# Optimization experiments

Hardware: AMD Instinct MI355X
Metric: run time of the kernel (lower is better)

## Reference

```python
import jax, jax.numpy as jnp
import numpy as np

N_NODES = 50000
N_EDGES = 800000
N_GRAPHS = 1000
IN_F = 11
H = 128
BN_EPS = 1e-5


def _bn(h, g, b):
    # BatchNorm1d training-mode math (biased variance), no running stats
    m = h.mean(axis=0)
    v = h.var(axis=0)
    return (h - m) * jax.lax.rsqrt(v + BN_EPS) * g + b


def _mlp(h, w1, b1, g1, be1, w2, b2, g2, be2):
    h = jax.nn.relu(_bn(h @ w1 + b1, g1, be1))
    h = jax.nn.relu(_bn(h @ w2 + b2, g2, be2))
    return h


def _gin_agg(h, edge_index):
    # GINConv with eps=0: (1+eps)*x + sum_{j->i} x_j
    msgs = h[edge_index[0]]  # [E, F] gather
    agg = jax.ops.segment_sum(msgs, edge_index[1], num_segments=N_NODES)
    return h + agg


def setup_inputs() -> dict:
    key = jax.random.key(0)
    ks = jax.random.split(key, 24)
    d = {}
    d["x"] = jax.random.normal(ks[0], (N_NODES, IN_F), dtype=jnp.float32)
    d["edge_index"] = jax.random.randint(ks[1], (2, N_EDGES), 0, N_NODES, dtype=jnp.int64)
    d["batch"] = jnp.sort(jax.random.randint(ks[2], (N_NODES,), 0, N_GRAPHS, dtype=jnp.int64))

    dims = [
        ("l1", IN_F, H), ("l2", H, H),            # conv1 MLP
        ("l3", H, 2 * H), ("l4", 2 * H, 2 * H),    # conv2 MLP
        ("l5", 2 * H, 2 * H), ("l6", 2 * H, 2 * H),# conv3 MLP
    ]
    ki = 3
    for name, fi, fo in dims:
        d[name + "w"] = jax.random.normal(ks[ki], (fi, fo), dtype=jnp.float32) * (1.0 / np.sqrt(fi)); ki += 1
        d[name + "b"] = jax.random.normal(ks[ki], (fo,), dtype=jnp.float32) * 0.02; ki += 1
        d[name + "g"] = 1.0 + jax.random.normal(ks[ki], (fo,), dtype=jnp.float32) * 0.02; ki += 1
        d[name + "be"] = jax.random.normal(ks[ki], (fo,), dtype=jnp.float32) * 0.02; ki += 1
        ks = jax.random.split(ks[-1], 24); ki = 0
    d["fw1"] = jax.random.normal(ks[0], (2 * H, H), dtype=jnp.float32) * (1.0 / np.sqrt(2 * H))
    d["fb1"] = jax.random.normal(ks[1], (H,), dtype=jnp.float32) * 0.02
    d["fg"] = 1.0 + jax.random.normal(ks[2], (H,), dtype=jnp.float32) * 0.02
    d["fbe"] = jax.random.normal(ks[3], (H,), dtype=jnp.float32) * 0.02
    d["fw2"] = jax.random.normal(ks[4], (H, 1), dtype=jnp.float32) * (1.0 / np.sqrt(H))
    d["fb2"] = jax.random.normal(ks[5], (1,), dtype=jnp.float32) * 0.02
    return d


def reference(x, edge_index, batch,
              l1w, l1b, l1g, l1be, l2w, l2b, l2g, l2be,
              l3w, l3b, l3g, l3be, l4w, l4b, l4g, l4be,
              l5w, l5b, l5g, l5be, l6w, l6b, l6g, l6be,
              fw1, fb1, fg, fbe, fw2, fb2):
    # conv1 + relu (dropout = identity in eval)
    h = _mlp(_gin_agg(x, edge_index), l1w, l1b, l1g, l1be, l2w, l2b, l2g, l2be)
    h = jax.nn.relu(h)
    # conv2 + relu
    h = _mlp(_gin_agg(h, edge_index), l3w, l3b, l3g, l3be, l4w, l4b, l4g, l4be)
    h = jax.nn.relu(h)
    # conv3 + relu
    h = _mlp(_gin_agg(h, edge_index), l5w, l5b, l5g, l5be, l6w, l6b, l6g, l6be)
    h = jax.nn.relu(h)
    # global_add_pool over graphs
    hg = jax.ops.segment_sum(h, batch, num_segments=N_GRAPHS)  # [G, 256]
    hg = jax.nn.relu(_bn(hg @ fw1 + fb1, fg, fbe))
    out = hg @ fw2 + fb2  # [G, 1]
    return out.reshape(-1)
```

## Files before the change

kernel.cpp:

```cpp
#include <hip/hip_runtime.h>

#define NNODES 50000
#define NEDGES 800000
#define NGRAPHS 1000
#define BN_EPS 1e-5f
#define MPAD 50048

typedef unsigned short us_t;
typedef us_t us8 __attribute__((ext_vector_type(8)));
typedef us_t us4 __attribute__((ext_vector_type(4)));
typedef __bf16 bf16x8 __attribute__((ext_vector_type(8)));
typedef float f32x4 __attribute__((ext_vector_type(4)));

__device__ __forceinline__ float b2f(us_t u) {
    union { unsigned int i; float f; } v;
    v.i = ((unsigned int)u) << 16;
    return v.f;
}
__device__ __forceinline__ us_t f2b(float x) {
    unsigned int u = __float_as_uint(x);
    unsigned int r = u + 0x7FFFu + ((u >> 16) & 1u);
    return (us_t)(r >> 16);
}
__device__ __forceinline__ float h2f(us_t u) {
    _Float16 h;
    __builtin_memcpy(&h, &u, 2);
    return (float)h;
}
__device__ __forceinline__ us_t f2h(float x) {
    _Float16 h = (_Float16)x;
    us_t u;
    __builtin_memcpy(&u, &h, 2);
    return u;
}
__device__ __forceinline__ bf16x8 as_bf(us8 v) {
    union { us8 u; bf16x8 b; } c;
    c.u = v;
    return c.b;
}

__device__ __forceinline__ void glds16(const us_t* g, us_t* l) {
    __builtin_amdgcn_global_load_lds(
        (const __attribute__((address_space(1))) void*)g,
        (__attribute__((address_space(3))) void*)l, 16, 0, 0);
}


__global__ void zero_f32(float* __restrict__ p, int n) {
    int i = blockIdx.x * blockDim.x + threadIdx.x;
    if (i < n) p[i] = 0.f;
}


__global__ void csr_hist(const int* __restrict__ dst, int* __restrict__ deg, int E) {
    int e = blockIdx.x * blockDim.x + threadIdx.x;
    if (e < E) atomicAdd(&deg[dst[e]], 1);
}

__global__ void csr_scan1(const int* __restrict__ deg, int* __restrict__ tmpscan,
                          int* __restrict__ chunkTot, int n) {
    __shared__ int sm[1024];
    int i = blockIdx.x * 1024 + threadIdx.x;
    int v = (i < n) ? deg[i] : 0;
    sm[threadIdx.x] = v;
    __syncthreads();
    for (int off = 1; off < 1024; off <<= 1) {
        int add = (threadIdx.x >= off) ? sm[threadIdx.x - off] : 0;
        __syncthreads();
        sm[threadIdx.x] += add;
        __syncthreads();
    }
    if (i < n) tmpscan[i] = sm[threadIdx.x];
    if (threadIdx.x == 1023) chunkTot[blockIdx.x] = sm[1023];
}

__global__ void csr_scan2(int* __restrict__ chunkTot, int nchunks) {
    if (threadIdx.x == 0 && blockIdx.x == 0) {
        int run = 0;
        for (int c = 0; c < nchunks; c++) {
            int t = chunkTot[c];
            chunkTot[c] = run;
            run += t;
        }
    }
}

__global__ void csr_scan3(const int* __restrict__ deg, const int* __restrict__ tmpscan,
                          const int* __restrict__ chunkTot, int* __restrict__ rowptr,
                          int* __restrict__ cursor, int n) {
    int i = blockIdx.x * blockDim.x + threadIdx.x;
    if (i < n) {
        int inc = tmpscan[i] + chunkTot[i >> 10];
        rowptr[i + 1] = inc;
        cursor[i] = inc - deg[i];
        if (i == 0) rowptr[0] = 0;
    }
}

__global__ void csr_fill(const int* __restrict__ src, const int* __restrict__ dst,
                         int* __restrict__ cursor, int* __restrict__ eidx, int E) {
    int e = blockIdx.x * blockDim.x + threadIdx.x;
    if (e < E) {
        int pos = atomicAdd(&cursor[dst[e]], 1);
        eidx[pos] = src[e];
    }
}


__global__ void wt_convert_all(const float* __restrict__ w2, const float* __restrict__ w3,
                               const float* __restrict__ w4, const float* __restrict__ w5,
                               const float* __restrict__ w6,
                               us_t* __restrict__ o2, us_t* __restrict__ o3,
                               us_t* __restrict__ o4, us_t* __restrict__ o5,
                               us_t* __restrict__ o6) {
    int i = blockIdx.x * blockDim.x + threadIdx.x;
    if (i < 16384) {
        int k = i >> 7, n = i & 127;
        o2[n * 128 + k] = f2b(w2[i]);
    } else if (i < 49152) {
        int j = i - 16384; int k = j >> 8, n = j & 255;
        o3[n * 128 + k] = f2b(w3[j]);
    } else if (i < 114688) {
        int j = i - 49152; int k = j >> 8, n = j & 255;
        o4[n * 256 + k] = f2b(w4[j]);
    } else if (i < 180224) {
        int j = i - 114688; int k = j >> 8, n = j & 255;
        o5[n * 256 + k] = f2b(w5[j]);
    } else if (i < 245760) {
        int j = i - 180224; int k = j >> 8, n = j & 255;
        o6[n * 256 + k] = f2b(w6[j]);
    }
}


__global__ void gin_gather_bn128(const us_t* __restrict__ z, const float* __restrict__ sums,
                                 const float* __restrict__ sumsq, const float* __restrict__ gw,
                                 const float* __restrict__ bw, float invM,
                                 const int* __restrict__ rowptr, const int* __restrict__ eidx,
                                 us_t* __restrict__ out) {
    int ln = threadIdx.x >> 4;
    int fp = threadIdx.x & 15;
    int n = blockIdx.x * 16 + ln;
    if (n >= NNODES) return;
    int f0 = fp * 8;
    float s[8], t[8];
    #pragma unroll
    for (int q = 0; q < 8; q++) {
        float m = sums[f0 + q] * invM;
        float va = sumsq[f0 + q] * invM - m * m;
        s[q] = gw[f0 + q] * rsqrtf(va + BN_EPS);
        t[q] = bw[f0 + q] - m * s[q];
    }
    const us_t* zf = z + f0;
    float a[8];
    us8 v = *(const us8*)&zf[(size_t)n * 128];
    #pragma unroll
    for (int q = 0; q < 8; q++) a[q] = fmaxf(0.f, b2f(v[q]) * s[q] + t[q]);
    int p0 = rowptr[n], p1 = rowptr[n + 1];
    int p = p0;
    for (; p + 4 <= p1; p += 4) {
        int e0 = eidx[p], e1 = eidx[p + 1], e2 = eidx[p + 2], e3 = eidx[p + 3];
        us8 u0 = *(const us8*)&zf[(size_t)e0 * 128];
        us8 u1 = *(const us8*)&zf[(size_t)e1 * 128];
        us8 u2 = *(const us8*)&zf[(size_t)e2 * 128];
        us8 u3 = *(const us8*)&zf[(size_t)e3 * 128];
        #pragma unroll
        for (int q = 0; q < 8; q++)
            a[q] += fmaxf(0.f, b2f(u0[q]) * s[q] + t[q]) +
                    fmaxf(0.f, b2f(u1[q]) * s[q] + t[q]) +
                    fmaxf(0.f, b2f(u2[q]) * s[q] + t[q]) +
                    fmaxf(0.f, b2f(u3[q]) * s[q] + t[q]);
    }
    for (; p < p1; p++) {
        us8 u = *(const us8*)&zf[(size_t)eidx[p] * 128];
        #pragma unroll
        for (int q = 0; q < 8; q++) a[q] += fmaxf(0.f, b2f(u[q]) * s[q] + t[q]);
    }
    us8 o;
    #pragma unroll
    for (int q = 0; q < 8; q++) o[q] = f2b(a[q]);
    *(us8*)&out[(size_t)n * 128 + f0] = o;
}


__global__ void gin_gather_bn256(const us_t* __restrict__ z, const float* __restrict__ sums,
                                 const float* __restrict__ sumsq, const float* __restrict__ gw,
                                 const float* __restrict__ bw, float invM,
                                 const int* __restrict__ rowptr, const int* __restrict__ eidx,
                                 us_t* __restrict__ out) {
    int ln = threadIdx.x >> 5;
    int fp = threadIdx.x & 31;
    int n = blockIdx.x * 8 + ln;
    if (n >= NNODES) return;
    int f0 = fp * 8;
    float s[8], t[8];
    #pragma unroll
    for (int q = 0; q < 8; q++) {
        float m = sums[f0 + q] * invM;
        float va = sumsq[f0 + q] * invM - m * m;
        s[q] = gw[f0 + q] * rsqrtf(va + BN_EPS);
        t[q] = bw[f0 + q] - m * s[q];
    }
    const us_t* zf = z + f0;
    float a[8];
    us8 v = *(const us8*)&zf[(size_t)n * 256];
    #pragma unroll
    for (int q = 0; q < 8; q++) a[q] = fmaxf(0.f, b2f(v[q]) * s[q] + t[q]);
    int p0 = rowptr[n], p1 = rowptr[n + 1];
    int p = p0;
    for (; p + 4 <= p1; p += 4) {
        int e0 = eidx[p], e1 = eidx[p + 1], e2 = eidx[p + 2], e3 = eidx[p + 3];
        us8 u0 = *(const us8*)&zf[(size_t)e0 * 256];
        us8 u1 = *(const us8*)&zf[(size_t)e1 * 256];
        us8 u2 = *(const us8*)&zf[(size_t)e2 * 256];
        us8 u3 = *(const us8*)&zf[(size_t)e3 * 256];
        #pragma unroll
        for (int q = 0; q < 8; q++)
            a[q] += fmaxf(0.f, b2f(u0[q]) * s[q] + t[q]) +
                    fmaxf(0.f, b2f(u1[q]) * s[q] + t[q]) +
                    fmaxf(0.f, b2f(u2[q]) * s[q] + t[q]) +
                    fmaxf(0.f, b2f(u3[q]) * s[q] + t[q]);
    }
    for (; p < p1; p++) {
        us8 u = *(const us8*)&zf[(size_t)eidx[p] * 256];
        #pragma unroll
        for (int q = 0; q < 8; q++) a[q] += fmaxf(0.f, b2f(u[q]) * s[q] + t[q]);
    }
    us8 o;
    #pragma unroll
    for (int q = 0; q < 8; q++) o[q] = f2b(a[q]);
    *(us8*)&out[(size_t)n * 256 + f0] = o;
}

__global__ void gin_gather11(const float* __restrict__ x, const int* __restrict__ rowptr,
                             const int* __restrict__ eidx, float* __restrict__ out) {
    int local = threadIdx.x >> 4;
    int lane = threadIdx.x & 15;
    int n = blockIdx.x * 16 + local;
    if (n >= NNODES) return;
    int p0 = rowptr[n], p1 = rowptr[n + 1];
    float acc = (lane < 11) ? x[n * 11 + lane] : 0.f;
    for (int p = p0; p < p1; p++) {
        int src = eidx[p];
        if (lane < 11) acc += x[src * 11 + lane];
    }
    if (lane < 11) out[n * 11 + lane] = acc;
}


__global__ __launch_bounds__(256) void gemm11(const float* __restrict__ A,
                                              const float* __restrict__ W,
                                              const float* __restrict__ b,
                                              us_t* __restrict__ C,
                                              float* __restrict__ sums,
                                              float* __restrict__ sumsq) {
    __shared__ float sW[11 * 128];
    __shared__ float sArows[64 * 11];
    int tid = threadIdx.x;
    for (int i = tid; i < 11 * 128; i += 256) sW[i] = W[i];
    int r0 = blockIdx.x * 64;
    for (int i = tid; i < 64 * 11; i += 256) {
        int r = i / 11, c = i - r * 11;
        sArows[i] = (r0 + r < NNODES) ? A[(r0 + r) * 11 + c] : 0.f;
    }
    __syncthreads();
    int col = tid & 127;
    int half = tid >> 7;
    float bias = b[col];
    float cs = 0.f, cq = 0.f;
    for (int rr = half * 32; rr < half * 32 + 32; rr++) {
        int row = r0 + rr;
        if (row < NNODES) {
            float acc = bias;
            #pragma unroll
            for (int k = 0; k < 11; k++) acc += sArows[rr * 11 + k] * sW[k * 128 + col];
            C[(size_t)row * 128 + col] = f2h(acc);
            cs += acc;
            cq += acc * acc;
        }
    }
    __syncthreads();
    sArows[tid] = cs;
    sArows[256 + tid] = cq;
    __syncthreads();
    if (tid < 128) {
        atomicAdd(&sums[tid], sArows[tid] + sArows[tid + 128]);
        atomicAdd(&sumsq[tid], sArows[256 + tid] + sArows[256 + tid + 128]);
    }
}


template <int K_, int AMODE, int OMODE, int COLS>
__global__ __launch_bounds__(256, 4) void gemm_v7(
    const void* __restrict__ Ap, const us_t* __restrict__ Wt,
    const float* __restrict__ bias,
    const float* __restrict__ sums_in, const float* __restrict__ sumsq_in,
    const float* __restrict__ gma, const float* __restrict__ bet, float invM,
    void* __restrict__ Cp, float* __restrict__ sums, float* __restrict__ sumsq,
    int M, int N, int nrows) {
    __shared__ us_t sA[128 * 32];
    __shared__ us_t sB[128 * 32];
    __shared__ float sST[(AMODE >= 1) ? 2 * K_ : 2];

    int rowblk, colblk;
    if (COLS == 1) {
        rowblk = blockIdx.x;
        colblk = 0;
    } else {
        int g = blockIdx.x;
        rowblk = (g >> 4) * 8 + (g & 7);
        colblk = (g >> 3) & 1;
        if (rowblk >= nrows) return;
    }
    const int bm = rowblk * 128;
    const int bn = colblk * 128;

    const int tid = threadIdx.x;
    const int lane = tid & 63;
    const int wave = tid >> 6;
    const int wm = wave >> 1, wn = wave & 1;
    const int lrow = lane & 15, lquad = lane >> 4;

    if (AMODE >= 1) {
        if (tid < K_) {
            float m = sums_in[tid] * invM;
            float va = sumsq_in[tid] * invM - m * m;
            float sc = gma[tid] * rsqrtf(va + BN_EPS);
            sST[tid] = sc;
            sST[K_ + tid] = bet[tid] - m * sc;
        }
        __syncthreads();
    }

    f32x4 acc[4][4] = {};

    const int r0c = tid >> 2, q0c = tid & 3;
    const int r1c = (tid + 256) >> 2, q1c = tid & 3;

    #pragma unroll
    for (int kt = 0; kt < K_ / 32; kt++) {
        const int k0 = kt * 32;

        us8 pk[2];
        if (AMODE >= 1) {
            #pragma unroll
            for (int i = 0; i < 2; i++) {
                int row = (i == 0) ? r0c : r1c;
                int kq = (i == 0) ? q0c : q1c;
                int kk = k0 + kq * 8;
                float v[8];
                if (AMODE == 1) {
                    const float* ar = &((const float*)Ap)[(size_t)(bm + row) * K_ + kk];
                    float4 v0 = *(const float4*)ar;
                    float4 v1 = *(const float4*)(ar + 4);
                    v[0] = v0.x; v[1] = v0.y; v[2] = v0.z; v[3] = v0.w;
                    v[4] = v1.x; v[5] = v1.y; v[6] = v1.z; v[7] = v1.w;
                } else {
                    us8 u = *(const us8*)&((const us_t*)Ap)[(size_t)(bm + row) * K_ + kk];
                    #pragma unroll
                    for (int q = 0; q < 8; q++) v[q] = h2f(u[q]);
                }
                float4 s0 = *(const float4*)&sST[kk];
                float4 s1 = *(const float4*)&sST[kk + 4];
                float4 t0 = *(const float4*)&sST[K_ + kk];
                float4 t1 = *(const float4*)&sST[K_ + kk + 4];
                us8 o;
                o[0] = f2b(fmaxf(0.f, v[0] * s0.x + t0.x));
                o[1] = f2b(fmaxf(0.f, v[1] * s0.y + t0.y));
                o[2] = f2b(fmaxf(0.f, v[2] * s0.z + t0.z));
                o[3] = f2b(fmaxf(0.f, v[3] * s0.w + t0.w));
                o[4] = f2b(fmaxf(0.f, v[4] * s1.x + t1.x));
                o[5] = f2b(fmaxf(0.f, v[5] * s1.y + t1.y));
                o[6] = f2b(fmaxf(0.f, v[6] * s1.z + t1.z));
                o[7] = f2b(fmaxf(0.f, v[7] * s1.w + t1.w));
                pk[i] = o;
            }
        }

        __syncthreads();

        {
            glds16(&Wt[(size_t)(bn + r0c) * K_ + k0 + q0c * 8], &sB[(wave * 64) * 8]);
            glds16(&Wt[(size_t)(bn + r1c) * K_ + k0 + q1c * 8], &sB[(256 + wave * 64) * 8]);
        }
        if (AMODE == 0) {
            const us_t* A = (const us_t*)Ap;
            glds16(&A[(size_t)(bm + r0c) * K_ + k0 + q0c * 8], &sA[(wave * 64) * 8]);
            glds16(&A[(size_t)(bm + r1c) * K_ + k0 + q1c * 8], &sA[(256 + wave * 64) * 8]);
        } else {
            *(us8*)&sA[(size_t)tid * 8] = pk[0];
            *(us8*)&sA[(size_t)(tid + 256) * 8] = pk[1];
        }

        __syncthreads();

        bf16x8 af[4], bfr[4];
        #pragma unroll
        for (int i = 0; i < 4; i++)
            af[i] = as_bf(*(const us8*)&sA[(wm * 64 + i * 16 + lrow) * 32 + lquad * 8]);
        #pragma unroll
        for (int j = 0; j < 4; j++)
            bfr[j] = as_bf(*(const us8*)&sB[(wn * 64 + j * 16 + lrow) * 32 + lquad * 8]);
        #pragma unroll
        for (int i = 0; i < 4; i++)
            #pragma unroll
            for (int j = 0; j < 4; j++)
                acc[i][j] = __builtin_amdgcn_mfma_f32_16x16x32_bf16(af[i], bfr[j],
                                                                    acc[i][j], 0, 0, 0);
    }

    #pragma unroll
    for (int j = 0; j < 4; j++) {
        int col = bn + wn * 64 + j * 16 + lrow;
        float bcol = bias[col];
        float cs = 0.f, cq = 0.f;
        #pragma unroll
        for (int i = 0; i < 4; i++) {
            int rb = bm + wm * 64 + i * 16 + lquad * 4;
            #pragma unroll
            for (int r = 0; r < 4; r++) {
                int row = rb + r;
                float zv = acc[i][j][r] + bcol;
                if (row < M) {
                    if (OMODE == 0)
                        ((us_t*)Cp)[(size_t)row * N + col] = f2b(zv);
                    else if (OMODE == 1)
                        ((float*)Cp)[(size_t)row * N + col] = zv;
                    else
                        ((us_t*)Cp)[(size_t)row * N + col] = f2h(zv);
                    cs += zv;
                    cq += zv * zv;
                }
            }
        }
        cs += __shfl_xor(cs, 16); cs += __shfl_xor(cs, 32);
        cq += __shfl_xor(cq, 16); cq += __shfl_xor(cq, 32);
        if (lquad == 0) {
            atomicAdd(&sums[col], cs);
            atomicAdd(&sumsq[col], cq);
        }
    }
}


__global__ void pool_bn_raw(const float* __restrict__ z, const float* __restrict__ sums,
                            const float* __restrict__ sumsq, const float* __restrict__ gw,
                            const float* __restrict__ bw, float invM,
                            const int* __restrict__ batch, float* __restrict__ hg) {
    int f = threadIdx.x;
    float m = sums[f] * invM;
    float va = sumsq[f] * invM - m * m;
    float sv = gw[f] * rsqrtf(va + BN_EPS);
    float tv = bw[f] - m * sv;
    int n0 = blockIdx.x * 32;
    int n1 = min(n0 + 32, NNODES);
    float acc = 0.f;
    int gc = batch[n0];
    for (int n = n0; n < n1; n++) {
        int g = batch[n];
        if (g != gc) {
            atomicAdd(&hg[gc * 256 + f], acc);
            acc = 0.f;
            gc = g;
        }
        acc += fmaxf(0.f, z[(size_t)n * 256 + f] * sv + tv);
    }
    atomicAdd(&hg[gc * 256 + f], acc);
}


#define GBM 128
#define GBN 128
#define GBK 16
#define LDA 132

__global__ __launch_bounds__(256) void gemm_f32_head(
    const float* __restrict__ A, const float* __restrict__ W, const float* __restrict__ bias,
    float* __restrict__ C, float* __restrict__ sums, float* __restrict__ sumsq,
    int M, int K, int N) {
    __shared__ float smem[2 * GBK * LDA];
    float* As = smem;
    float* Ws = smem + GBK * LDA;

    const int bm = blockIdx.y * GBM;
    const int bn = blockIdx.x * GBN;
    const int tid = threadIdx.x;
    const int tm = tid >> 4;
    const int tn = tid & 15;

    float acc[2][2][4][4] = {};

    for (int k0 = 0; k0 < K; k0 += GBK) {
        #pragma unroll
        for (int i = 0; i < 2; i++) {
            int id = tid + 256 * i;
            int row = id >> 2;
            int kq = id & 3;
            int gr = bm + row;
            int kk = k0 + kq * 4;
            float4 a4 = make_float4(0.f, 0.f, 0.f, 0.f);
            if (gr < M && kk < K) a4 = *(const float4*)&A[(size_t)gr * K + kk];
            As[(kq * 4 + 0) * LDA + row] = a4.x;
            As[(kq * 4 + 1) * LDA + row] = a4.y;
            As[(kq * 4 + 2) * LDA + row] = a4.z;
            As[(kq * 4 + 3) * LDA + row] = a4.w;
        }
        #pragma unroll
        for (int i = 0; i < 2; i++) {
            int id = tid + 256 * i;
            int kl = id >> 5;
            int c = id & 31;
            int kk = k0 + kl;
            float4 w4 = make_float4(0.f, 0.f, 0.f, 0.f);
            if (kk < K && bn + c * 4 < N) w4 = *(const float4*)&W[(size_t)kk * N + bn + c * 4];
            *(float4*)&Ws[kl * LDA + c * 4] = w4;
        }
        __syncthreads();
        #pragma unroll
        for (int k = 0; k < GBK; k++) {
            float4 a0 = *(float4*)&As[k * LDA + tm * 4];
            float4 a1 = *(float4*)&As[k * LDA + 64 + tm * 4];
            float4 w0 = *(float4*)&Ws[k * LDA + tn * 4];
            float4 w1 = *(float4*)&Ws[k * LDA + 64 + tn * 4];
            float ar[2][4] = {{a0.x, a0.y, a0.z, a0.w}, {a1.x, a1.y, a1.z, a1.w}};
            float wr[2][4] = {{w0.x, w0.y, w0.z, w0.w}, {w1.x, w1.y, w1.z, w1.w}};
            #pragma unroll
            for (int ri = 0; ri < 2; ri++)
                #pragma unroll
                for (int ci = 0; ci < 2; ci++)
                    #pragma unroll
                    for (int ii = 0; ii < 4; ii++)
                        #pragma unroll
                        for (int jj = 0; jj < 4; jj++)
                            acc[ri][ci][ii][jj] += ar[ri][ii] * wr[ci][jj];
        }
        __syncthreads();
    }

    float colsum[2][4] = {};
    float colsq[2][4] = {};
    #pragma unroll
    for (int ci = 0; ci < 2; ci++) {
        int colbase = bn + ci * 64 + tn * 4;
        if (colbase >= N) continue;
        float4 b4 = *(const float4*)&bias[colbase];
        float br[4] = {b4.x, b4.y, b4.z, b4.w};
        #pragma unroll
        for (int ri = 0; ri < 2; ri++) {
            #pragma unroll
            for (int ii = 0; ii < 4; ii++) {
                int row = bm + ri * 64 + tm * 4 + ii;
                if (row < M) {
                    float z0 = acc[ri][ci][ii][0] + br[0];
                    float z1 = acc[ri][ci][ii][1] + br[1];
                    float z2 = acc[ri][ci][ii][2] + br[2];
                    float z3 = acc[ri][ci][ii][3] + br[3];
                    *(float4*)&C[(size_t)row * N + colbase] = make_float4(z0, z1, z2, z3);
                    colsum[ci][0] += z0; colsq[ci][0] += z0 * z0;
                    colsum[ci][1] += z1; colsq[ci][1] += z1 * z1;
                    colsum[ci][2] += z2; colsq[ci][2] += z2 * z2;
                    colsum[ci][3] += z3; colsq[ci][3] += z3 * z3;
                }
            }
        }
    }
    __syncthreads();
    float* ps = smem;
    float* pq = smem + 2048;
    #pragma unroll
    for (int ci = 0; ci < 2; ci++)
        #pragma unroll
        for (int jj = 0; jj < 4; jj++) {
            int cl = ci * 64 + tn * 4 + jj;
            ps[tm * 128 + cl] = colsum[ci][jj];
            pq[tm * 128 + cl] = colsq[ci][jj];
        }
    __syncthreads();
    if (tid < 128 && bn + tid < N) {
        float s = 0.f, q = 0.f;
        #pragma unroll
        for (int i = 0; i < 16; i++) {
            s += ps[i * 128 + tid];
            q += pq[i * 128 + tid];
        }
        atomicAdd(&sums[bn + tid], s);
        atomicAdd(&sumsq[bn + tid], q);
    }
}


__global__ void final_gemv_raw(const float* __restrict__ hg2, const float* __restrict__ sums,
                               const float* __restrict__ sumsq, const float* __restrict__ gw,
                               const float* __restrict__ bw, float invM,
                               const float* __restrict__ fw2, const float* __restrict__ fb2,
                               float* __restrict__ out) {
    int g = blockIdx.x;
    int l = threadIdx.x;
    float m0 = sums[l] * invM, va0 = sumsq[l] * invM - m0 * m0;
    float s0 = gw[l] * rsqrtf(va0 + BN_EPS), t0 = bw[l] - m0 * s0;
    float m1 = sums[64 + l] * invM, va1 = sumsq[64 + l] * invM - m1 * m1;
    float s1 = gw[64 + l] * rsqrtf(va1 + BN_EPS), t1 = bw[64 + l] - m1 * s1;
    float a0 = fmaxf(0.f, hg2[g * 128 + l] * s0 + t0) * fw2[l];
    float a1 = fmaxf(0.f, hg2[g * 128 + 64 + l] * s1 + t1) * fw2[64 + l];
    float v = a0 + a1;
    #pragma unroll
    for (int o = 32; o > 0; o >>= 1) v += __shfl_down(v, o);
    if (l == 0) out[g] = v + fb2[0];
}


extern "C" void kernel_launch(void* const* d_in, const int* in_sizes, int n_in,
                              void* d_out, int out_size, void* d_ws, size_t ws_size,
                              hipStream_t stream) {
    const float* x = (const float*)d_in[0];
    const int* ei = (const int*)d_in[1];
    const int* batch = (const int*)d_in[2];
    const int* esrc = ei;
    const int* edst = ei + NEDGES;

    const float* l1w = (const float*)d_in[3],  *l1b = (const float*)d_in[4],
               * l1g = (const float*)d_in[5],  *l1be = (const float*)d_in[6];
    const float* l2w = (const float*)d_in[7],  *l2b = (const float*)d_in[8],
               * l2g = (const float*)d_in[9],  *l2be = (const float*)d_in[10];
    const float* l3w = (const float*)d_in[11], *l3b = (const float*)d_in[12],
               * l3g = (const float*)d_in[13], *l3be = (const float*)d_in[14];
    const float* l4w = (const float*)d_in[15], *l4b = (const float*)d_in[16],
               * l4g = (const float*)d_in[17], *l4be = (const float*)d_in[18];
    const float* l5w = (const float*)d_in[19], *l5b = (const float*)d_in[20],
               * l5g = (const float*)d_in[21], *l5be = (const float*)d_in[22];
    const float* l6w = (const float*)d_in[23], *l6b = (const float*)d_in[24],
               * l6g = (const float*)d_in[25], *l6be = (const float*)d_in[26];
    const float* fw1 = (const float*)d_in[27], *fb1 = (const float*)d_in[28],
               * fg  = (const float*)d_in[29], *fbe = (const float*)d_in[30];
    const float* fw2 = (const float*)d_in[31], *fb2 = (const float*)d_in[32];

    us_t* F0h = (us_t*)d_ws;
    float* F1 = (float*)(F0h + (size_t)MPAD * 256);
    us_t* Ba = (us_t*)F1;
    us_t* Bz = Ba + (size_t)MPAD * 256;
    us_t* wt2 = (us_t*)(F1 + (size_t)MPAD * 256);
    us_t* wt3 = wt2 + 128 * 128;
    us_t* wt4 = wt3 + 256 * 128;
    us_t* wt5 = wt4 + 256 * 256;
    us_t* wt6 = wt5 + 256 * 256;
    float* agg11 = (float*)(wt6 + 256 * 256);
    float* hg = agg11 + (size_t)NNODES * 11;
    float* hg2 = hg + NGRAPHS * 256;
    float* stats = hg2 + NGRAPHS * 128;
    int* deg = (int*)(stats + 7 * 512);
    int* rowptr = deg + (NNODES + 1);
    int* cursor = rowptr + (NNODES + 1);
    int* chunkTot = cursor + (NNODES + 1);
    int* tmpscan = chunkTot + 64;
    int* eidx = tmpscan + (NNODES + 1);

    {
        int zn = NGRAPHS * 256 + NGRAPHS * 128 + 7 * 512 + (NNODES + 1);
        zero_f32<<<(zn + 255) / 256, 256, 0, stream>>>(hg, zn);
    }

    csr_hist<<<(NEDGES + 255) / 256, 256, 0, stream>>>(edst, deg, NEDGES);
    int nchunks = (NNODES + 1023) / 1024;
    csr_scan1<<<nchunks, 1024, 0, stream>>>(deg, tmpscan, chunkTot, NNODES);
    csr_scan2<<<1, 64, 0, stream>>>(chunkTot, nchunks);
    csr_scan3<<<(NNODES + 255) / 256, 256, 0, stream>>>(deg, tmpscan, chunkTot, rowptr,
                                                        cursor, NNODES);
    csr_fill<<<(NEDGES + 255) / 256, 256, 0, stream>>>(esrc, edst, cursor, eidx, NEDGES);

    wt_convert_all<<<(245760 + 255) / 256, 256, 0, stream>>>(l2w, l3w, l4w, l5w, l6w,
                                                             wt2, wt3, wt4, wt5, wt6);

    auto st = [&](int i) { return stats + i * 512; };
    const float invN = 1.0f / (float)NNODES;
    const float invG = 1.0f / (float)NGRAPHS;
    const int NRB = MPAD / 128;
    const int NSWZ = ((NRB + 7) / 8) * 16;

    gin_gather11<<<(NNODES + 15) / 16, 256, 0, stream>>>(x, rowptr, eidx, agg11);
    gemm11<<<(NNODES + 63) / 64, 256, 0, stream>>>(agg11, l1w, l1b, F0h, st(0), st(0) + 256);
    gemm_v7<128, 2, 0, 1><<<NRB, 256, 0, stream>>>(
        F0h, wt2, l2b, st(0), st(0) + 256, l1g, l1be, invN,
        Bz, st(1), st(1) + 256, NNODES, 128, NRB);

    gin_gather_bn128<<<(NNODES + 15) / 16, 256, 0, stream>>>(
        Bz, st(1), st(1) + 256, l2g, l2be, invN, rowptr, eidx, Ba);
    gemm_v7<128, 0, 2, 2><<<NSWZ, 256, 0, stream>>>(
        Ba, wt3, l3b, nullptr, nullptr, nullptr, nullptr, 0.f,
        F0h, st(2), st(2) + 256, NNODES, 256, NRB);
    gemm_v7<256, 2, 0, 2><<<NSWZ, 256, 0, stream>>>(
        F0h, wt4, l4b, st(2), st(2) + 256, l3g, l3be, invN,
        Bz, st(3), st(3) + 256, NNODES, 256, NRB);

    gin_gather_bn256<<<(NNODES + 7) / 8, 256, 0, stream>>>(
        Bz, st(3), st(3) + 256, l4g, l4be, invN, rowptr, eidx, Ba);
    gemm_v7<256, 0, 2, 2><<<NSWZ, 256, 0, stream>>>(
        Ba, wt5, l5b, nullptr, nullptr, nullptr, nullptr, 0.f,
        F0h, st(4), st(4) + 256, NNODES, 256, NRB);
    gemm_v7<256, 2, 1, 2><<<NSWZ, 256, 0, stream>>>(
        F0h, wt6, l6b, st(4), st(4) + 256, l5g, l5be, invN,
        F1, st(5), st(5) + 256, NNODES, 256, NRB);

    pool_bn_raw<<<(NNODES + 31) / 32, 256, 0, stream>>>(
        F1, st(5), st(5) + 256, l6g, l6be, invN, batch, hg);
    gemm_f32_head<<<dim3(1, 8), 256, 0, stream>>>(hg, fw1, fb1, hg2, st(6), st(6) + 256,
                                                  NGRAPHS, 256, 128);
    final_gemv_raw<<<NGRAPHS, 64, 0, stream>>>(hg2, st(6), st(6) + 256, fg, fbe, invG,
                                               fw2, fb2, (float*)d_out);
}
```

Before: 626.9 us.

## Stage GEMM epilogue through LDS for vectorized stores; store last layer in fp16

The GEMM epilogue now writes the biased outputs into shared memory, one half-tile of 64 rows at a time, and then copies them out with 16-byte coalesced row stores. Before, each thread wrote scattered 2-byte elements straight to global memory. The last MLP layer now writes fp16 instead of fp32, so the pooling kernel reads half the bytes. The cost is two extra barriers per half-tile, LDS reuse, and lower precision on the final activations before BN and pooling.

```diff
diff --git a/kernel.cpp b/kernel.cpp
--- a/kernel.cpp
+++ b/kernel.cpp
@@ -291,16 +291,17 @@
 
 
 template <int K_, int AMODE, int OMODE, int COLS>
-__global__ __launch_bounds__(256, 4) void gemm_v7(
+__global__ __launch_bounds__(256, 4) void gemm_v8(
     const void* __restrict__ Ap, const us_t* __restrict__ Wt,
     const float* __restrict__ bias,
     const float* __restrict__ sums_in, const float* __restrict__ sumsq_in,
     const float* __restrict__ gma, const float* __restrict__ bet, float invM,
-    void* __restrict__ Cp, float* __restrict__ sums, float* __restrict__ sumsq,
+    us_t* __restrict__ Cp, float* __restrict__ sums, float* __restrict__ sumsq,
     int M, int N, int nrows) {
-    __shared__ us_t sA[128 * 32];
-    __shared__ us_t sB[128 * 32];
+    __shared__ us_t sAB[2 * 128 * 32];
     __shared__ float sST[(AMODE >= 1) ? 2 * K_ : 2];
+    us_t* sA = sAB;
+    us_t* sB = sAB + 128 * 32;
 
     int rowblk, colblk;
     if (COLS == 1) {
@@ -419,15 +420,8 @@
             int rb = bm + wm * 64 + i * 16 + lquad * 4;
             #pragma unroll
             for (int r = 0; r < 4; r++) {
-                int row = rb + r;
-                float zv = acc[i][j][r] + bcol;
-                if (row < M) {
-                    if (OMODE == 0)
-                        ((us_t*)Cp)[(size_t)row * N + col] = f2b(zv);
-                    else if (OMODE == 1)
-                        ((float*)Cp)[(size_t)row * N + col] = zv;
-                    else
-                        ((us_t*)Cp)[(size_t)row * N + col] = f2h(zv);
+                if (rb + r < M) {
+                    float zv = acc[i][j][r] + bcol;
                     cs += zv;
                     cq += zv * zv;
                 }
@@ -440,13 +434,44 @@
             atomicAdd(&sumsq[col], cq);
         }
     }
-}
-
-
-__global__ void pool_bn_raw(const float* __restrict__ z, const float* __restrict__ sums,
-                            const float* __restrict__ sumsq, const float* __restrict__ gw,
-                            const float* __restrict__ bw, float invM,
-                            const int* __restrict__ batch, float* __restrict__ hg) {
+
+    #pragma unroll
+    for (int p = 0; p < 2; p++) {
+        __syncthreads();
+        if (wm == p) {
+            #pragma unroll
+            for (int j = 0; j < 4; j++) {
+                int coll = wn * 64 + j * 16 + lrow;
+                float bcol = bias[bn + coll];
+                #pragma unroll
+                for (int i = 0; i < 4; i++) {
+                    int rl = i * 16 + lquad * 4;
+                    #pragma unroll
+                    for (int r = 0; r < 4; r++) {
+                        float zv = acc[i][j][r] + bcol;
+                        sAB[(rl + r) * 128 + coll] = (OMODE == 0) ? f2b(zv) : f2h(zv);
+                    }
+                }
+            }
+        }
+        __syncthreads();
+        #pragma unroll
+        for (int k = 0; k < 4; k++) {
+            int c = tid + 256 * k;
+            int row = c >> 4, cw = c & 15;
+            int grow = bm + p * 64 + row;
+            if (grow < M)
+                *(us8*)&Cp[(size_t)grow * N + bn + cw * 8] =
+                    *(const us8*)&sAB[row * 128 + cw * 8];
+        }
+    }
+}
+
+
+__global__ void pool_bn_h(const us_t* __restrict__ z, const float* __restrict__ sums,
+                          const float* __restrict__ sumsq, const float* __restrict__ gw,
+                          const float* __restrict__ bw, float invM,
+                          const int* __restrict__ batch, float* __restrict__ hg) {
     int f = threadIdx.x;
     float m = sums[f] * invM;
     float va = sumsq[f] * invM - m * m;
@@ -463,7 +488,7 @@
             acc = 0.f;
             gc = g;
         }
-        acc += fmaxf(0.f, z[(size_t)n * 256 + f] * sv + tv);
+        acc += fmaxf(0.f, h2f(z[(size_t)n * 256 + f]) * sv + tv);
     }
     atomicAdd(&hg[gc * 256 + f], acc);
 }
@@ -635,10 +660,9 @@
     const float* fw2 = (const float*)d_in[31], *fb2 = (const float*)d_in[32];
 
     us_t* F0h = (us_t*)d_ws;
-    float* F1 = (float*)(F0h + (size_t)MPAD * 256);
-    us_t* Ba = (us_t*)F1;
+    us_t* Ba = F0h + (size_t)MPAD * 256;
     us_t* Bz = Ba + (size_t)MPAD * 256;
-    us_t* wt2 = (us_t*)(F1 + (size_t)MPAD * 256);
+    us_t* wt2 = Bz + (size_t)MPAD * 256;
     us_t* wt3 = wt2 + 128 * 128;
     us_t* wt4 = wt3 + 256 * 128;
     us_t* wt5 = wt4 + 256 * 256;
@@ -678,30 +702,30 @@
 
     gin_gather11<<<(NNODES + 15) / 16, 256, 0, stream>>>(x, rowptr, eidx, agg11);
     gemm11<<<(NNODES + 63) / 64, 256, 0, stream>>>(agg11, l1w, l1b, F0h, st(0), st(0) + 256);
-    gemm_v7<128, 2, 0, 1><<<NRB, 256, 0, stream>>>(
+    gemm_v8<128, 2, 0, 1><<<NRB, 256, 0, stream>>>(
         F0h, wt2, l2b, st(0), st(0) + 256, l1g, l1be, invN,
         Bz, st(1), st(1) + 256, NNODES, 128, NRB);
 
     gin_gather_bn128<<<(NNODES + 15) / 16, 256, 0, stream>>>(
         Bz, st(1), st(1) + 256, l2g, l2be, invN, rowptr, eidx, Ba);
-    gemm_v7<128, 0, 2, 2><<<NSWZ, 256, 0, stream>>>(
+    gemm_v8<128, 0, 2, 2><<<NSWZ, 256, 0, stream>>>(
         Ba, wt3, l3b, nullptr, nullptr, nullptr, nullptr, 0.f,
         F0h, st(2), st(2) + 256, NNODES, 256, NRB);
-    gemm_v7<256, 2, 0, 2><<<NSWZ, 256, 0, stream>>>(
+    gemm_v8<256, 2, 0, 2><<<NSWZ, 256, 0, stream>>>(
         F0h, wt4, l4b, st(2), st(2) + 256, l3g, l3be, invN,
         Bz, st(3), st(3) + 256, NNODES, 256, NRB);
 
     gin_gather_bn256<<<(NNODES + 7) / 8, 256, 0, stream>>>(
         Bz, st(3), st(3) + 256, l4g, l4be, invN, rowptr, eidx, Ba);
-    gemm_v7<256, 0, 2, 2><<<NSWZ, 256, 0, stream>>>(
+    gemm_v8<256, 0, 2, 2><<<NSWZ, 256, 0, stream>>>(
         Ba, wt5, l5b, nullptr, nullptr, nullptr, nullptr, 0.f,
         F0h, st(4), st(4) + 256, NNODES, 256, NRB);
-    gemm_v7<256, 2, 1, 2><<<NSWZ, 256, 0, stream>>>(
+    gemm_v8<256, 2, 2, 2><<<NSWZ, 256, 0, stream>>>(
         F0h, wt6, l6b, st(4), st(4) + 256, l5g, l5be, invN,
-        F1, st(5), st(5) + 256, NNODES, 256, NRB);
-
-    pool_bn_raw<<<(NNODES + 31) / 32, 256, 0, stream>>>(
-        F1, st(5), st(5) + 256, l6g, l6be, invN, batch, hg);
+        Bz, st(5), st(5) + 256, NNODES, 256, NRB);
+
+    pool_bn_h<<<(NNODES + 31) / 32, 256, 0, stream>>>(
+        Bz, st(5), st(5) + 256, l6g, l6be, invN, batch, hg);
     gemm_f32_head<<<dim3(1, 8), 256, 0, stream>>>(hg, fw1, fb1, hg2, st(6), st(6) + 256,
                                                   NGRAPHS, 256, 128);
     final_gemv_raw<<<NGRAPHS, 64, 0, stream>>>(hg2, st(6), st(6) + 256, fg, fbe, invG,
```

Result: faster. 600.7 us (-4.2%).
